# Performance work log

Measured on AMD Instinct MI355X. Metric: run time of the kernel, lower is better.

Reference implementation:

```python
import jax, jax.numpy as jnp
import numpy as np

D_MODEL = 1024
N_EXPERTS = 16384
N_HEADS = 8
TOP_K = 16
D_KEY = 128
N_SUB = int(np.sqrt(N_EXPERTS))  # 128
BN_EPS = 1e-5
RMS_EPS = 1e-6


def setup_inputs() -> dict:
    key = jax.random.key(0)
    ks = jax.random.split(key, 12)
    b, t = 2, 512
    hk = N_HEADS * D_KEY  # 1024
    s = 0.02
    return {
        "x": jax.random.normal(ks[0], (b, t, D_MODEL), dtype=jnp.float32),
        "wq": jax.random.normal(ks[1], (hk, D_MODEL), dtype=jnp.float32) * s,
        "bq": jnp.zeros((hk,), dtype=jnp.float32),
        "bn_w": jnp.ones((hk,), dtype=jnp.float32),
        "bn_b": jnp.zeros((hk,), dtype=jnp.float32),
        "bn_mean": jnp.zeros((hk,), dtype=jnp.float32),
        "bn_var": jnp.ones((hk,), dtype=jnp.float32),
        "sub_keys": jax.random.normal(ks[2], (2, N_SUB, D_KEY // 2), dtype=jnp.float32),
        "expert_weights": jax.random.normal(ks[3], (N_EXPERTS, D_KEY), dtype=jnp.float32),
        "wo": jax.random.normal(ks[4], (D_MODEL, hk), dtype=jnp.float32) * s,
        "bo": jnp.zeros((D_MODEL,), dtype=jnp.float32),
        "in_proj_w": jax.random.normal(ks[5], (3 * D_MODEL, D_MODEL), dtype=jnp.float32) * s,
        "in_proj_b": jnp.zeros((3 * D_MODEL,), dtype=jnp.float32),
        "attn_ow": jax.random.normal(ks[6], (D_MODEL, D_MODEL), dtype=jnp.float32) * s,
        "attn_ob": jnp.zeros((D_MODEL,), dtype=jnp.float32),
        "rms_w": jnp.ones((D_MODEL,), dtype=jnp.float32),
    }


def reference(x, wq, bq, bn_w, bn_b, bn_mean, bn_var, sub_keys, expert_weights,
              wo, bo, in_proj_w, in_proj_b, attn_ow, attn_ob, rms_w):
    b, t, d = x.shape
    h, dk = N_HEADS, D_KEY

    # ---- PEER query path ----
    q = jnp.einsum('btd,ed->bte', x, wq) + bq                       # (b,t,h*dk)
    # BatchNorm1d in eval mode with running stats
    q = (q - bn_mean) * jax.lax.rsqrt(bn_var + BN_EPS) * bn_w + bn_b
    q = q.reshape(b, t, h, dk)

    # ---- product-key top-k retrieval ----
    q1, q2 = q[..., : dk // 2], q[..., dk // 2 :]
    s1 = jnp.einsum('bthc,nc->bthn', q1, sub_keys[0])               # (b,t,h,N_SUB)
    s2 = jnp.einsum('bthc,nc->bthn', q2, sub_keys[1])
    # cartesian add; flat index = i1*N_SUB + i2 (matches torch view)
    scores = (s1[..., :, None] + s2[..., None, :]).reshape(b, t, h, N_SUB * N_SUB)
    _, idx = jax.lax.top_k(scores, TOP_K)                           # (b,t,h,k)

    # ---- gather experts, router softmax, weighted sum ----
    ew = expert_weights[idx]                                        # (b,t,h,k,dk)
    sim = jnp.einsum('bthd,bthkd->bthk', q, ew)
    rw = jax.nn.softmax(sim, axis=-1)
    out = jnp.einsum('bthk,bthkd->bthd', rw, ew).reshape(b, t, h * dk)
    out = jnp.einsum('bte,de->btd', out, wo) + bo                   # (b,t,d)

    # ---- multihead self-attention (torch nn.MultiheadAttention semantics) ----
    hd = d // h
    qkv = jnp.einsum('btd,ed->bte', x, in_proj_w) + in_proj_b       # (b,t,3d)
    qa, ka, va = jnp.split(qkv, 3, axis=-1)
    def heads(z):
        return z.reshape(b, t, h, hd).transpose(0, 2, 1, 3)         # (b,h,t,hd)
    qa, ka, va = heads(qa), heads(ka), heads(va)
    att = jax.nn.softmax(jnp.einsum('bhqe,bhke->bhqk', qa, ka) / np.sqrt(hd), axis=-1)
    ao = jnp.einsum('bhqk,bhke->bhqe', att, va).transpose(0, 2, 1, 3).reshape(b, t, d)
    ao = jnp.einsum('btd,ed->bte', ao, attn_ow) + attn_ob
    attn_weights = att.mean(axis=1)                                 # (b,t,t), averaged over heads

    # ---- residual + RMSNorm ----
    y = x + out + ao
    y = y * jax.lax.rsqrt(jnp.mean(y * y, axis=-1, keepdims=True) + RMS_EPS) * rms_w
    return y, attn_weights
```

## Files before the change

### kernel.cpp

```cpp
#include <hip/hip_runtime.h>
#include <hip/hip_bf16.h>
#include <math.h>

typedef __attribute__((ext_vector_type(8))) short bf16x8;
typedef __attribute__((ext_vector_type(4))) float f32x4;

__device__ inline short f2bf(float f) {
    __hip_bfloat16 h = __float2bfloat16(f);
    return *reinterpret_cast<short*>(&h);
}

__device__ inline unsigned int obits(float f) {
    unsigned int u = __float_as_uint(f);
    return (u & 0x80000000u) ? ~u : (u | 0x80000000u);
}

__global__ __launch_bounds__(256) void gemm_mfma64(
    const float* __restrict__ A, long lda, long sAb, long sAh,
    const float* __restrict__ B, long ldb, long sBb, long sBh,
    float* __restrict__ C, long ldc, long sCb, long sCh,
    int K, const float* __restrict__ bias, float scale, int hDiv)
{
    int bz = blockIdx.z;
    int bb = bz / hDiv, hh = bz % hDiv;
    A += bb * sAb + hh * sAh;
    B += bb * sBb + hh * sBh;
    C += bb * sCb + hh * sCh;
    int bm = blockIdx.y * 64, bn = blockIdx.x * 64;

    __shared__ __align__(16) short Asub[2048];
    __shared__ __align__(16) short Bsub[2048];

    int tid = threadIdx.x;
    int lane = tid & 63;
    int wave = tid >> 6;
    int wr = wave >> 1, wc = wave & 1;
    int l15 = lane & 15, l4 = lane >> 4;

    f32x4 acc[2][2] = {};

    int sr = tid >> 2;
    int sq = tid & 3;
    const float* gA = A + (long)(bm + sr) * lda + sq * 8;
    const float* gB = B + (long)(bn + sr) * ldb + sq * 8;
    short* wA = Asub + (sr >> 4) * 512 + sq * 128 + (sr & 15) * 8;
    short* wB = Bsub + (sr >> 4) * 512 + sq * 128 + (sr & 15) * 8;

    float4 a0 = *(const float4*)(gA);
    float4 a1 = *(const float4*)(gA + 4);
    float4 b0 = *(const float4*)(gB);
    float4 b1 = *(const float4*)(gB + 4);

    for (int k0 = 0; k0 < K; k0 += 32) {
        bf16x8 ua, ub;
        ua[0]=f2bf(a0.x); ua[1]=f2bf(a0.y); ua[2]=f2bf(a0.z); ua[3]=f2bf(a0.w);
        ua[4]=f2bf(a1.x); ua[5]=f2bf(a1.y); ua[6]=f2bf(a1.z); ua[7]=f2bf(a1.w);
        ub[0]=f2bf(b0.x); ub[1]=f2bf(b0.y); ub[2]=f2bf(b0.z); ub[3]=f2bf(b0.w);
        ub[4]=f2bf(b1.x); ub[5]=f2bf(b1.y); ub[6]=f2bf(b1.z); ub[7]=f2bf(b1.w);
        *(bf16x8*)wA = ua;
        *(bf16x8*)wB = ub;
        __syncthreads();

        if (k0 + 32 < K) {
            a0 = *(const float4*)(gA + k0 + 32);
            a1 = *(const float4*)(gA + k0 + 36);
            b0 = *(const float4*)(gB + k0 + 32);
            b1 = *(const float4*)(gB + k0 + 36);
        }

        bf16x8 af[2], bfr[2];
#pragma unroll
        for (int mi = 0; mi < 2; mi++)
            af[mi] = *(const bf16x8*)(Asub + (wr * 2 + mi) * 512 + l4 * 128 + l15 * 8);
#pragma unroll
        for (int ni = 0; ni < 2; ni++)
            bfr[ni] = *(const bf16x8*)(Bsub + (wc * 2 + ni) * 512 + l4 * 128 + l15 * 8);
#pragma unroll
        for (int mi = 0; mi < 2; mi++)
#pragma unroll
            for (int ni = 0; ni < 2; ni++)
                acc[mi][ni] = __builtin_amdgcn_mfma_f32_16x16x32_bf16(
                    af[mi], bfr[ni], acc[mi][ni], 0, 0, 0);
        __syncthreads();
    }

#pragma unroll
    for (int ni = 0; ni < 2; ni++) {
        int c = bn + wc * 32 + ni * 16 + l15;
        float bv = bias ? bias[c] : 0.f;
#pragma unroll
        for (int mi = 0; mi < 2; mi++) {
            int r0 = bm + wr * 32 + mi * 16 + l4 * 4;
#pragma unroll
            for (int e = 0; e < 4; e++)
                C[(long)(r0 + e) * ldc + c] = acc[mi][ni][e] * scale + bv;
        }
    }
}

__global__ __launch_bounds__(256) void sgemm_qproj(
    const float* __restrict__ A, const float* __restrict__ W,
    float* __restrict__ Q,
    const float* __restrict__ bq, const float* __restrict__ bn_w,
    const float* __restrict__ bn_b, const float* __restrict__ bn_mean,
    const float* __restrict__ bn_var)
{
    int bm = blockIdx.y * 64, bn = blockIdx.x * 64;
    __shared__ float As[32][64];
    __shared__ float Bs[32][64];
    int tid = threadIdx.x;
    int tx = tid & 15, ty = tid >> 4;
    int r = tid >> 2, q4 = tid & 3;
    float acc[4][4] = {{0.f}};

    const float* ga = A + (long)(bm + r) * 1024 + q4 * 8;
    const float* gb = W + (long)(bn + r) * 1024 + q4 * 8;

    float4 a0 = *(const float4*)(ga);
    float4 a1 = *(const float4*)(ga + 4);
    float4 b0 = *(const float4*)(gb);
    float4 b1 = *(const float4*)(gb + 4);

    for (int k0 = 0; k0 < 1024; k0 += 32) {
        __syncthreads();
        As[q4 * 8 + 0][r] = a0.x; As[q4 * 8 + 1][r] = a0.y;
        As[q4 * 8 + 2][r] = a0.z; As[q4 * 8 + 3][r] = a0.w;
        As[q4 * 8 + 4][r] = a1.x; As[q4 * 8 + 5][r] = a1.y;
        As[q4 * 8 + 6][r] = a1.z; As[q4 * 8 + 7][r] = a1.w;
        Bs[q4 * 8 + 0][r] = b0.x; Bs[q4 * 8 + 1][r] = b0.y;
        Bs[q4 * 8 + 2][r] = b0.z; Bs[q4 * 8 + 3][r] = b0.w;
        Bs[q4 * 8 + 4][r] = b1.x; Bs[q4 * 8 + 5][r] = b1.y;
        Bs[q4 * 8 + 6][r] = b1.z; Bs[q4 * 8 + 7][r] = b1.w;
        if (k0 + 32 < 1024) {
            a0 = *(const float4*)(ga + k0 + 32);
            a1 = *(const float4*)(ga + k0 + 36);
            b0 = *(const float4*)(gb + k0 + 32);
            b1 = *(const float4*)(gb + k0 + 36);
        }
        __syncthreads();
#pragma unroll
        for (int kk = 0; kk < 32; kk++) {
            float4 av = *(const float4*)&As[kk][ty * 4];
            float4 bv = *(const float4*)&Bs[kk][tx * 4];
            float a[4] = {av.x, av.y, av.z, av.w};
            float b[4] = {bv.x, bv.y, bv.z, bv.w};
#pragma unroll
            for (int i = 0; i < 4; i++)
#pragma unroll
                for (int j = 0; j < 4; j++)
                    acc[i][j] = fmaf(a[i], b[j], acc[i][j]);
        }
    }

#pragma unroll
    for (int j = 0; j < 4; j++) {
        int n = bn + tx * 4 + j;
        float s = rsqrtf(bn_var[n] + 1e-5f) * bn_w[n];
        float base = bq[n] - bn_mean[n];
        float bb = bn_b[n];
#pragma unroll
        for (int i = 0; i < 4; i++) {
            long m = bm + ty * 4 + i;
            Q[m * 1024 + n] = (acc[i][j] + base) * s + bb;
        }
    }
}

__global__ __launch_bounds__(256) void transpose_va(
    const float* __restrict__ qkv, float* __restrict__ vat)
{
    int z = blockIdx.z;
    int b = z >> 3, h = z & 7;
    int k0 = blockIdx.x * 32, n0 = blockIdx.y * 32;
    __shared__ float tile[32][33];
    int tx = threadIdx.x & 31, ty = threadIdx.x >> 5;
    const float* src = qkv + 2048 + (long)b * 1572864 + (long)h * 128;
#pragma unroll
    for (int i = 0; i < 4; i++)
        tile[ty + 8 * i][tx] = src[(long)(k0 + ty + 8 * i) * 3072 + n0 + tx];
    __syncthreads();
    float* dst = vat + (long)z * 65536;
#pragma unroll
    for (int i = 0; i < 4; i++)
        dst[(long)(n0 + ty + 8 * i) * 512 + k0 + tx] = tile[tx][ty + 8 * i];
}

__global__ __launch_bounds__(128) void peer_kernel(
    const float* __restrict__ q,
    const float* __restrict__ sub_keys,
    const float* __restrict__ ew,
    float* __restrict__ out)
{
    int th = blockIdx.x;
    int tid = threadIdx.x;

    __shared__ __align__(16) float qrow[128];
    __shared__ __align__(16) unsigned long long k1s[128];
    __shared__ __align__(16) unsigned long long k2s[128];
    __shared__ __align__(16) unsigned long long cks[256];
    __shared__ float tv1[16], tv2[16];
    __shared__ int   ti1[16], ti2[16];
    __shared__ int   part[100];
    __shared__ int   eid[16];
    __shared__ float simv[16];
    __shared__ float rw[16];

    qrow[tid] = q[(long)th * 128 + tid];
    __syncthreads();

    float a1, a2;
    {
        const float4* k1 = (const float4*)(sub_keys + tid * 64);
        const float4* k2 = (const float4*)(sub_keys + 8192 + tid * 64);
        float s1 = 0.f, s2 = 0.f;
#pragma unroll 4
        for (int c = 0; c < 16; c++) {
            float4 v1 = k1[c], v2 = k2[c];
            s1 = fmaf(qrow[4 * c + 0], v1.x, s1);
            s1 = fmaf(qrow[4 * c + 1], v1.y, s1);
            s1 = fmaf(qrow[4 * c + 2], v1.z, s1);
            s1 = fmaf(qrow[4 * c + 3], v1.w, s1);
            s2 = fmaf(qrow[64 + 4 * c + 0], v2.x, s2);
            s2 = fmaf(qrow[64 + 4 * c + 1], v2.y, s2);
            s2 = fmaf(qrow[64 + 4 * c + 2], v2.z, s2);
            s2 = fmaf(qrow[64 + 4 * c + 3], v2.w, s2);
        }
        a1 = s1; a2 = s2;
    }
    unsigned long long key1 = ((unsigned long long)obits(a1) << 32) | (unsigned)(127 - tid);
    unsigned long long key2 = ((unsigned long long)obits(a2) << 32) | (unsigned)(127 - tid);
    k1s[tid] = key1;
    k2s[tid] = key2;
    __syncthreads();

    {
        int r1 = 0, r2 = 0;
#pragma unroll 4
        for (int j = 0; j < 128; j++) {
            r1 += (k1s[j] > key1);
            r2 += (k2s[j] > key2);
        }
        if (r1 < 16) { tv1[r1] = a1; ti1[r1] = tid; }
        if (r2 < 16) { tv2[r2] = a2; ti2[r2] = tid; }
    }
    __syncthreads();

    {
        int c0 = tid, c1 = tid + 128;
        float s0 = tv1[c0 >> 4] + tv2[c0 & 15];
        int e0 = ti1[c0 >> 4] * 128 + ti2[c0 & 15];
        cks[c0] = ((unsigned long long)obits(s0) << 32) | (unsigned)(16383 - e0);
        float s1v = tv1[c1 >> 4] + tv2[c1 & 15];
        int e1 = ti1[c1 >> 4] * 128 + ti2[c1 & 15];
        cks[c1] = ((unsigned long long)obits(s1v) << 32) | (unsigned)(16383 - e1);
    }
    __syncthreads();

    if (tid < 100) {
        int c = tid >> 1, h = tid & 1;
        int i, j;
        if      (c < 16) { i = 0; j = c; }
        else if (c < 24) { i = 1; j = c - 16; }
        else if (c < 29) { i = 2; j = c - 24; }
        else if (c < 33) { i = 3; j = c - 29; }
        else if (c < 36) { i = 4; j = c - 33; }
        else if (c < 38) { i = 5; j = c - 36; }
        else if (c < 40) { i = 6; j = c - 38; }
        else if (c < 42) { i = 7; j = c - 40; }
        else             { i = 8 + (c - 42); j = 0; }
        unsigned long long mk = cks[i * 16 + j];
        const unsigned long long* base = cks + h * 128;
        int cnt = 0;
#pragma unroll 4
        for (int t = 0; t < 128; t++) cnt += (base[t] > mk);
        part[tid] = cnt;
    }
    __syncthreads();
    if (tid < 50) {
        int r = part[2 * tid] + part[2 * tid + 1];
        if (r < 16) {
            int c = tid;
            int i, j;
            if      (c < 16) { i = 0; j = c; }
            else if (c < 24) { i = 1; j = c - 16; }
            else if (c < 29) { i = 2; j = c - 24; }
            else if (c < 33) { i = 3; j = c - 29; }
            else if (c < 36) { i = 4; j = c - 33; }
            else if (c < 38) { i = 5; j = c - 36; }
            else if (c < 40) { i = 6; j = c - 38; }
            else if (c < 42) { i = 7; j = c - 40; }
            else             { i = 8 + (c - 42); j = 0; }
            eid[r] = ti1[i] * 128 + ti2[j];
        }
    }
    __syncthreads();

    {
        int e = tid >> 3, g = tid & 7;
        const float4* e4 = (const float4*)(ew + (long)eid[e] * 128 + g * 16);
        const float* qb = qrow + g * 16;
        float acc = 0.f;
#pragma unroll 2
        for (int m = 0; m < 4; m++) {
            float4 v = e4[m];
            acc = fmaf(qb[4 * m + 0], v.x, acc);
            acc = fmaf(qb[4 * m + 1], v.y, acc);
            acc = fmaf(qb[4 * m + 2], v.z, acc);
            acc = fmaf(qb[4 * m + 3], v.w, acc);
        }
        acc += __shfl_down(acc, 4);
        acc += __shfl_down(acc, 2);
        acc += __shfl_down(acc, 1);
        if (g == 0) simv[e] = acc;
    }
    __syncthreads();

    if (tid < 16) {
        float mx = simv[0];
#pragma unroll
        for (int k = 1; k < 16; k++) mx = fmaxf(mx, simv[k]);
        rw[tid] = expf(simv[tid] - mx);
    }
    __syncthreads();

    {
        float wsum = 0.f;
#pragma unroll
        for (int k = 0; k < 16; k++) wsum += rw[k];
        float inv = 1.f / wsum;
        float o = 0.f;
#pragma unroll
        for (int k = 0; k < 16; k++)
            o = fmaf(rw[k], ew[(long)eid[k] * 128 + tid], o);
        out[(long)th * 128 + tid] = o * inv;
    }
}

__global__ __launch_bounds__(256) void softmax_mean(
    float* __restrict__ att, float* __restrict__ outw)
{
    int blk = blockIdx.x;
    int b = blk >> 9, row = blk & 511;
    int tid = threadIdx.x;
    int w = tid >> 6, lane = tid & 63;

    __shared__ float msum[4][516];

#pragma unroll
    for (int pass = 0; pass < 2; pass++) {
        int h = w + pass * 4;
        long base = ((long)(b * 8 + h) * 512 + row) * 512 + lane * 8;
        float4 v0 = *(const float4*)(att + base);
        float4 v1 = *(const float4*)(att + base + 4);
        float m = fmaxf(fmaxf(fmaxf(v0.x, v0.y), fmaxf(v0.z, v0.w)),
                        fmaxf(fmaxf(v1.x, v1.y), fmaxf(v1.z, v1.w)));
#pragma unroll
        for (int off = 32; off > 0; off >>= 1)
            m = fmaxf(m, __shfl_xor(m, off));
        float e[8];
        e[0] = expf(v0.x - m); e[1] = expf(v0.y - m);
        e[2] = expf(v0.z - m); e[3] = expf(v0.w - m);
        e[4] = expf(v1.x - m); e[5] = expf(v1.y - m);
        e[6] = expf(v1.z - m); e[7] = expf(v1.w - m);
        float s = e[0] + e[1] + e[2] + e[3] + e[4] + e[5] + e[6] + e[7];
#pragma unroll
        for (int off = 32; off > 0; off >>= 1)
            s += __shfl_xor(s, off);
        float inv = 1.f / s;
        float4 p0 = make_float4(e[0] * inv, e[1] * inv, e[2] * inv, e[3] * inv);
        float4 p1 = make_float4(e[4] * inv, e[5] * inv, e[6] * inv, e[7] * inv);
        *(float4*)(att + base) = p0;
        *(float4*)(att + base + 4) = p1;
        int c = lane * 8;
        if (pass == 0) {
            msum[w][c + 0] = p0.x; msum[w][c + 1] = p0.y;
            msum[w][c + 2] = p0.z; msum[w][c + 3] = p0.w;
            msum[w][c + 4] = p1.x; msum[w][c + 5] = p1.y;
            msum[w][c + 6] = p1.z; msum[w][c + 7] = p1.w;
        } else {
            msum[w][c + 0] += p0.x; msum[w][c + 1] += p0.y;
            msum[w][c + 2] += p0.z; msum[w][c + 3] += p0.w;
            msum[w][c + 4] += p1.x; msum[w][c + 5] += p1.y;
            msum[w][c + 6] += p1.z; msum[w][c + 7] += p1.w;
        }
    }
    __syncthreads();
#pragma unroll
    for (int i = 0; i < 2; i++) {
        int c = tid + i * 256;
        float s = (msum[0][c] + msum[1][c] + msum[2][c] + msum[3][c]) * 0.125f;
        outw[(long)blk * 512 + c] = s;
    }
}

__global__ __launch_bounds__(256) void final_fuse(
    const float* __restrict__ x, const float* __restrict__ out2,
    const float* __restrict__ ao2, const float* __restrict__ rms_w,
    float* __restrict__ y)
{
    long base = (long)blockIdx.x * 1024;
    int tid = threadIdx.x;
    float v[4];
    float ss = 0.f;
#pragma unroll
    for (int i = 0; i < 4; i++) {
        int d = tid + i * 256;
        v[i] = x[base + d] + out2[base + d] + ao2[base + d];
        ss = fmaf(v[i], v[i], ss);
    }
    __shared__ float red[256];
    red[tid] = ss;
    __syncthreads();
    for (int st = 128; st > 0; st >>= 1) {
        if (tid < st) red[tid] += red[tid + st];
        __syncthreads();
    }
    float scale = rsqrtf(red[0] * (1.f / 1024.f) + 1e-6f);
#pragma unroll
    for (int i = 0; i < 4; i++) {
        int d = tid + i * 256;
        y[base + d] = v[i] * scale * rms_w[d];
    }
}

extern "C" void kernel_launch(void* const* d_in, const int* in_sizes, int n_in,
                              void* d_out, int out_size, void* d_ws, size_t ws_size,
                              hipStream_t stream)
{
    const float* x         = (const float*)d_in[0];
    const float* wq        = (const float*)d_in[1];
    const float* bq        = (const float*)d_in[2];
    const float* bn_w      = (const float*)d_in[3];
    const float* bn_b      = (const float*)d_in[4];
    const float* bn_mean   = (const float*)d_in[5];
    const float* bn_var    = (const float*)d_in[6];
    const float* sub_keys  = (const float*)d_in[7];
    const float* ew        = (const float*)d_in[8];
    const float* wo        = (const float*)d_in[9];
    const float* bo        = (const float*)d_in[10];
    const float* in_proj_w = (const float*)d_in[11];
    const float* in_proj_b = (const float*)d_in[12];
    const float* attn_ow   = (const float*)d_in[13];
    const float* attn_ob   = (const float*)d_in[14];
    const float* rms_w     = (const float*)d_in[15];
    float* out = (float*)d_out;

    float* ws   = (float*)d_ws;
    float* q    = ws;
    float* peer = ws + 1048576;
    float* out2 = ws + 2097152;
    float* qkv  = ws + 3145728;
    float* att  = ws + 6291456;
    float* ao   = ws + 10485760;
    float* ao2  = ws + 11534336;
    float* vat  = q;

    dim3 blk(256);

    sgemm_qproj<<<dim3(16, 16, 1), blk, 0, stream>>>(
        x, wq, q, bq, bn_w, bn_b, bn_mean, bn_var);

    peer_kernel<<<8192, 128, 0, stream>>>(q, sub_keys, ew, peer);

    gemm_mfma64<<<dim3(16, 16, 1), blk, 0, stream>>>(
        peer, 1024L, 0L, 0L, wo, 1024L, 0L, 0L, out2, 1024L, 0L, 0L,
        1024, bo, 1.0f, 1);

    gemm_mfma64<<<dim3(48, 16, 1), blk, 0, stream>>>(
        x, 1024L, 0L, 0L, in_proj_w, 1024L, 0L, 0L, qkv, 3072L, 0L, 0L,
        1024, in_proj_b, 1.0f, 1);

    transpose_va<<<dim3(16, 4, 16), blk, 0, stream>>>(qkv, vat);

    gemm_mfma64<<<dim3(8, 8, 16), blk, 0, stream>>>(
        qkv, 3072L, 1572864L, 128L,
        qkv + 1024, 3072L, 1572864L, 128L,
        att, 512L, 2097152L, 262144L,
        128, nullptr, 0.08838834764831845f, 8);

    softmax_mean<<<1024, 256, 0, stream>>>(att, out + 1048576);

    gemm_mfma64<<<dim3(2, 8, 16), blk, 0, stream>>>(
        att, 512L, 2097152L, 262144L,
        vat, 512L, 524288L, 65536L,
        ao, 1024L, 524288L, 128L,
        512, nullptr, 1.0f, 8);

    gemm_mfma64<<<dim3(16, 16, 1), blk, 0, stream>>>(
        ao, 1024L, 0L, 0L, attn_ow, 1024L, 0L, 0L, ao2, 1024L, 0L, 0L,
        1024, attn_ob, 1.0f, 1);

    final_fuse<<<1024, 256, 0, stream>>>(x, out2, ao2, rms_w, out);
}
```

Before: 335.9 us.

## Double-buffer GEMM LDS tiles and vectorize PEER top-k shared reads

The bf16 MFMA GEMM now keeps two LDS buffers, so the next tile is converted and stored while the current one feeds the MFMAs. This removes one barrier per k-step and prefetches global loads two steps ahead. The PEER kernel ranks raw float scores with an explicit index tie-break instead of packed 64-bit keys, and reads shared memory as float4 and ulonglong2. The cost is double the LDS for the GEMM, plus float comparisons that must tie-break exactly like before.

```diff
diff --git a/kernel.cpp b/kernel.cpp
--- a/kernel.cpp
+++ b/kernel.cpp
@@ -28,8 +28,8 @@
     C += bb * sCb + hh * sCh;
     int bm = blockIdx.y * 64, bn = blockIdx.x * 64;
 
-    __shared__ __align__(16) short Asub[2048];
-    __shared__ __align__(16) short Bsub[2048];
+    __shared__ __align__(16) short Asub[2][2048];
+    __shared__ __align__(16) short Bsub[2][2048];
 
     int tid = threadIdx.x;
     int lane = tid & 63;
@@ -43,38 +43,55 @@
     int sq = tid & 3;
     const float* gA = A + (long)(bm + sr) * lda + sq * 8;
     const float* gB = B + (long)(bn + sr) * ldb + sq * 8;
-    short* wA = Asub + (sr >> 4) * 512 + sq * 128 + (sr & 15) * 8;
-    short* wB = Bsub + (sr >> 4) * 512 + sq * 128 + (sr & 15) * 8;
+    int woff = (sr >> 4) * 512 + sq * 128 + (sr & 15) * 8;
 
     float4 a0 = *(const float4*)(gA);
     float4 a1 = *(const float4*)(gA + 4);
     float4 b0 = *(const float4*)(gB);
     float4 b1 = *(const float4*)(gB + 4);
-
-    for (int k0 = 0; k0 < K; k0 += 32) {
+    {
         bf16x8 ua, ub;
         ua[0]=f2bf(a0.x); ua[1]=f2bf(a0.y); ua[2]=f2bf(a0.z); ua[3]=f2bf(a0.w);
         ua[4]=f2bf(a1.x); ua[5]=f2bf(a1.y); ua[6]=f2bf(a1.z); ua[7]=f2bf(a1.w);
         ub[0]=f2bf(b0.x); ub[1]=f2bf(b0.y); ub[2]=f2bf(b0.z); ub[3]=f2bf(b0.w);
         ub[4]=f2bf(b1.x); ub[5]=f2bf(b1.y); ub[6]=f2bf(b1.z); ub[7]=f2bf(b1.w);
-        *(bf16x8*)wA = ua;
-        *(bf16x8*)wB = ub;
-        __syncthreads();
+        *(bf16x8*)(Asub[0] + woff) = ua;
+        *(bf16x8*)(Bsub[0] + woff) = ub;
+    }
+    if (K > 32) {
+        a0 = *(const float4*)(gA + 32);
+        a1 = *(const float4*)(gA + 36);
+        b0 = *(const float4*)(gB + 32);
+        b1 = *(const float4*)(gB + 36);
+    }
+    __syncthreads();
+
+    int p = 0;
+    for (int k0 = 0; k0 < K; k0 += 32) {
+        bf16x8 af[2], bfr[2];
+#pragma unroll
+        for (int mi = 0; mi < 2; mi++)
+            af[mi] = *(const bf16x8*)(Asub[p] + (wr * 2 + mi) * 512 + l4 * 128 + l15 * 8);
+#pragma unroll
+        for (int ni = 0; ni < 2; ni++)
+            bfr[ni] = *(const bf16x8*)(Bsub[p] + (wc * 2 + ni) * 512 + l4 * 128 + l15 * 8);
 
         if (k0 + 32 < K) {
-            a0 = *(const float4*)(gA + k0 + 32);
-            a1 = *(const float4*)(gA + k0 + 36);
-            b0 = *(const float4*)(gB + k0 + 32);
-            b1 = *(const float4*)(gB + k0 + 36);
-        }
-
-        bf16x8 af[2], bfr[2];
-#pragma unroll
-        for (int mi = 0; mi < 2; mi++)
-            af[mi] = *(const bf16x8*)(Asub + (wr * 2 + mi) * 512 + l4 * 128 + l15 * 8);
-#pragma unroll
-        for (int ni = 0; ni < 2; ni++)
-            bfr[ni] = *(const bf16x8*)(Bsub + (wc * 2 + ni) * 512 + l4 * 128 + l15 * 8);
+            bf16x8 ua, ub;
+            ua[0]=f2bf(a0.x); ua[1]=f2bf(a0.y); ua[2]=f2bf(a0.z); ua[3]=f2bf(a0.w);
+            ua[4]=f2bf(a1.x); ua[5]=f2bf(a1.y); ua[6]=f2bf(a1.z); ua[7]=f2bf(a1.w);
+            ub[0]=f2bf(b0.x); ub[1]=f2bf(b0.y); ub[2]=f2bf(b0.z); ub[3]=f2bf(b0.w);
+            ub[4]=f2bf(b1.x); ub[5]=f2bf(b1.y); ub[6]=f2bf(b1.z); ub[7]=f2bf(b1.w);
+            *(bf16x8*)(Asub[p ^ 1] + woff) = ua;
+            *(bf16x8*)(Bsub[p ^ 1] + woff) = ub;
+            if (k0 + 64 < K) {
+                a0 = *(const float4*)(gA + k0 + 64);
+                a1 = *(const float4*)(gA + k0 + 68);
+                b0 = *(const float4*)(gB + k0 + 64);
+                b1 = *(const float4*)(gB + k0 + 68);
+            }
+        }
+
 #pragma unroll
         for (int mi = 0; mi < 2; mi++)
 #pragma unroll
@@ -82,6 +99,7 @@
                 acc[mi][ni] = __builtin_amdgcn_mfma_f32_16x16x32_bf16(
                     af[mi], bfr[ni], acc[mi][ni], 0, 0, 0);
         __syncthreads();
+        p ^= 1;
     }
 
 #pragma unroll
@@ -195,8 +213,8 @@
     int tid = threadIdx.x;
 
     __shared__ __align__(16) float qrow[128];
-    __shared__ __align__(16) unsigned long long k1s[128];
-    __shared__ __align__(16) unsigned long long k2s[128];
+    __shared__ __align__(16) float s1s[128];
+    __shared__ __align__(16) float s2s[128];
     __shared__ __align__(16) unsigned long long cks[256];
     __shared__ float tv1[16], tv2[16];
     __shared__ int   ti1[16], ti2[16];
@@ -208,37 +226,38 @@
     qrow[tid] = q[(long)th * 128 + tid];
     __syncthreads();
 
-    float a1, a2;
+    float a1 = 0.f, a2 = 0.f;
     {
         const float4* k1 = (const float4*)(sub_keys + tid * 64);
         const float4* k2 = (const float4*)(sub_keys + 8192 + tid * 64);
-        float s1 = 0.f, s2 = 0.f;
 #pragma unroll 4
         for (int c = 0; c < 16; c++) {
+            float4 q1 = *(const float4*)&qrow[4 * c];
+            float4 q2 = *(const float4*)&qrow[64 + 4 * c];
             float4 v1 = k1[c], v2 = k2[c];
-            s1 = fmaf(qrow[4 * c + 0], v1.x, s1);
-            s1 = fmaf(qrow[4 * c + 1], v1.y, s1);
-            s1 = fmaf(qrow[4 * c + 2], v1.z, s1);
-            s1 = fmaf(qrow[4 * c + 3], v1.w, s1);
-            s2 = fmaf(qrow[64 + 4 * c + 0], v2.x, s2);
-            s2 = fmaf(qrow[64 + 4 * c + 1], v2.y, s2);
-            s2 = fmaf(qrow[64 + 4 * c + 2], v2.z, s2);
-            s2 = fmaf(qrow[64 + 4 * c + 3], v2.w, s2);
-        }
-        a1 = s1; a2 = s2;
-    }
-    unsigned long long key1 = ((unsigned long long)obits(a1) << 32) | (unsigned)(127 - tid);
-    unsigned long long key2 = ((unsigned long long)obits(a2) << 32) | (unsigned)(127 - tid);
-    k1s[tid] = key1;
-    k2s[tid] = key2;
+            a1 = fmaf(q1.x, v1.x, a1); a1 = fmaf(q1.y, v1.y, a1);
+            a1 = fmaf(q1.z, v1.z, a1); a1 = fmaf(q1.w, v1.w, a1);
+            a2 = fmaf(q2.x, v2.x, a2); a2 = fmaf(q2.y, v2.y, a2);
+            a2 = fmaf(q2.z, v2.z, a2); a2 = fmaf(q2.w, v2.w, a2);
+        }
+    }
+    s1s[tid] = a1;
+    s2s[tid] = a2;
     __syncthreads();
 
     {
         int r1 = 0, r2 = 0;
-#pragma unroll 4
-        for (int j = 0; j < 128; j++) {
-            r1 += (k1s[j] > key1);
-            r2 += (k2s[j] > key2);
+        for (int j = 0; j < 128; j += 4) {
+            float4 a = *(const float4*)&s1s[j];
+            float4 b = *(const float4*)&s2s[j];
+            r1 += (a.x > a1) || (a.x == a1 && j + 0 < tid);
+            r1 += (a.y > a1) || (a.y == a1 && j + 1 < tid);
+            r1 += (a.z > a1) || (a.z == a1 && j + 2 < tid);
+            r1 += (a.w > a1) || (a.w == a1 && j + 3 < tid);
+            r2 += (b.x > a2) || (b.x == a2 && j + 0 < tid);
+            r2 += (b.y > a2) || (b.y == a2 && j + 1 < tid);
+            r2 += (b.z > a2) || (b.z == a2 && j + 2 < tid);
+            r2 += (b.w > a2) || (b.w == a2 && j + 3 < tid);
         }
         if (r1 < 16) { tv1[r1] = a1; ti1[r1] = tid; }
         if (r2 < 16) { tv2[r2] = a2; ti2[r2] = tid; }
@@ -269,10 +288,14 @@
         else if (c < 42) { i = 7; j = c - 40; }
         else             { i = 8 + (c - 42); j = 0; }
         unsigned long long mk = cks[i * 16 + j];
-        const unsigned long long* base = cks + h * 128;
+        const ulonglong2* base = (const ulonglong2*)(cks + h * 128);
         int cnt = 0;
 #pragma unroll 4
-        for (int t = 0; t < 128; t++) cnt += (base[t] > mk);
+        for (int t = 0; t < 64; t++) {
+            ulonglong2 kk = base[t];
+            cnt += (kk.x > mk);
+            cnt += (kk.y > mk);
+        }
         part[tid] = cnt;
     }
     __syncthreads();
@@ -298,15 +321,16 @@
     {
         int e = tid >> 3, g = tid & 7;
         const float4* e4 = (const float4*)(ew + (long)eid[e] * 128 + g * 16);
-        const float* qb = qrow + g * 16;
+        const float4* qb = (const float4*)(qrow + g * 16);
         float acc = 0.f;
-#pragma unroll 2
+#pragma unroll
         for (int m = 0; m < 4; m++) {
             float4 v = e4[m];
-            acc = fmaf(qb[4 * m + 0], v.x, acc);
-            acc = fmaf(qb[4 * m + 1], v.y, acc);
-            acc = fmaf(qb[4 * m + 2], v.z, acc);
-            acc = fmaf(qb[4 * m + 3], v.w, acc);
+            float4 qv = qb[m];
+            acc = fmaf(qv.x, v.x, acc);
+            acc = fmaf(qv.y, v.y, acc);
+            acc = fmaf(qv.z, v.z, acc);
+            acc = fmaf(qv.w, v.w, acc);
         }
         acc += __shfl_down(acc, 4);
         acc += __shfl_down(acc, 2);
```

Result: faster. 316.2 us (-5.9%).
